# Kernel optimization log

Hardware: AMD Instinct MI355X
Metric: run time of the kernel (lower is better)

The kernel has to match this reference:

```python
import jax, jax.numpy as jnp
import numpy as np

N_NODES = 50000
N_EDGES = 1000000
DIM = 3
NV = 32  # n_vec_in
NS = 32  # n_scalar_in


def setup_inputs() -> dict:
    key = jax.random.key(0)
    ks = jax.random.split(key, 16)
    inp = {
        "xn": jax.random.normal(ks[0], (N_NODES, DIM, NV), dtype=jnp.float32),
        "xn_attr": jax.random.normal(ks[1], (N_NODES, NS), dtype=jnp.float32),
        "xe_attr": jax.random.normal(ks[2], (N_EDGES,), dtype=jnp.float32),
        "xe_src": jax.random.randint(ks[3], (N_EDGES,), 0, N_NODES),
        "xe_dst": jax.random.randint(ks[4], (N_EDGES,), 0, N_NODES),
        # MixVecScalar params
        "ms_M": jax.random.normal(ks[5], (NV, NS), dtype=jnp.float32),
        "ms_w": jax.random.normal(ks[6], (1,), dtype=jnp.float32),
        # fc1 / fc2: Linear(1, NV) -> weight [NV] (flattened [NV,1]), bias [NV]
        "fc1_w": jax.random.normal(ks[7], (NV,), dtype=jnp.float32),
        "fc1_b": jax.random.normal(ks[8], (NV,), dtype=jnp.float32),
        "fc2_w": jax.random.normal(ks[9], (NV,), dtype=jnp.float32),
        "fc2_b": jax.random.normal(ks[10], (NV,), dtype=jnp.float32),
        # NodesToEdges MixVecVec
        "n2e_M1": jax.random.normal(ks[11], (NV, NV), dtype=jnp.float32),
        "n2e_M2": jax.random.normal(ks[12], (NV, NV), dtype=jnp.float32),
        # standalone MixVecVec
        "vv_M1": jax.random.normal(ks[13], (NV, NV), dtype=jnp.float32),
        "vv_M2": jax.random.normal(ks[14], (NV, NV), dtype=jnp.float32),
        # EdgesToNodes MixVecVec
        "e2n_M1": jax.random.normal(jax.random.fold_in(key, 101), (NV, NV), dtype=jnp.float32),
        "e2n_M2": jax.random.normal(jax.random.fold_in(key, 102), (NV, NV), dtype=jnp.float32),
    }
    return inp


def reference(xn, xn_attr, xe_attr, xe_src, xe_dst,
              ms_M, ms_w, fc1_w, fc1_b, fc2_w, fc2_b,
              n2e_M1, n2e_M2, vv_M1, vv_M2, e2n_M1, e2n_M2):
    n_nodes = xn.shape[0]

    # MixVecScalar: x3 = ((xn @ M) * xn_attr[:,None,:]) @ M.T; blend by angle
    x3 = jnp.einsum('ndv,vs->nds', xn, ms_M) * xn_attr[:, None, :]
    x3 = jnp.einsum('nds,vs->ndv', x3, ms_M)
    angle = 0.1 * ms_w  # shape [1]
    xn = jnp.cos(angle) * xn + jnp.sin(angle) * x3

    # fc1: silu(Linear(1->NV)(xe_attr))  -> per-edge weight [E, NV]
    W1 = jax.nn.silu(xe_attr[:, None] * fc1_w[None, :] + fc1_b[None, :])

    # NodesToEdges: gather, weight, mix
    xs = xn[xe_src]  # [E, DIM, NV]
    xd = xn[xe_dst]
    xe_grad = W1[:, None, :] * (xs - xd)
    xe_ave = W1[:, None, :] * (xs + xd) / 2.0
    xe = (jnp.einsum('edv,vw->edw', xe_grad, n2e_M1)
          + jnp.einsum('edv,vw->edw', xe_ave, n2e_M2)) / 2.0

    # MixVecVec(xe, xe) = xe @ (M1 + M2) / 2
    xe = jnp.einsum('edv,vw->edw', xe, (vv_M1 + vv_M2) / 2.0)

    # fc2 weight
    W2 = jax.nn.silu(xe_attr[:, None] * fc2_w[None, :] + fc2_b[None, :])

    # EdgesToNodes: weighted scatter-add to dst and src, then mix
    wxe = W2[:, None, :] * xe  # [E, DIM, NV]
    xn_1 = jax.ops.segment_sum(wxe, xe_dst, num_segments=n_nodes)
    xn_2 = jax.ops.segment_sum(wxe, xe_src, num_segments=n_nodes)
    xn_div = xn_1 - xn_2
    xn_ave = xn_1 + xn_2
    xn = (jnp.einsum('ndv,vw->ndw', xn_div, e2n_M1)
          + jnp.einsum('ndv,vw->ndw', xn_ave, e2n_M2)) / 2.0

    # ActivationVec: x * tanh(||x||_dim1)
    xnorm = jnp.linalg.norm(xn, axis=1)  # [N, NV]
    xn = xn * jnp.tanh(xnorm)[:, None, :]
    return xn
```

## Files before the change

### kernel.cpp

```cpp
#include <hip/hip_runtime.h>
#include <math.h>


typedef __attribute__((ext_vector_type(8))) short bf16x8;
typedef __attribute__((ext_vector_type(4))) float f32x4;

__device__ __forceinline__ float silu_f(float x) { return x / (1.0f + __expf(-x)); }

__device__ __forceinline__ unsigned cvt_pk_bf16(float lo, float hi) {
  unsigned r;
  asm("v_cvt_pk_bf16_f32 %0, %1, %2" : "=v"(r) : "v"(lo), "v"(hi));
  return r;
}
__device__ __forceinline__ float bf_lo(unsigned w) { return __uint_as_float(w << 16); }
__device__ __forceinline__ float bf_hi(unsigned w) { return __uint_as_float(w & 0xFFFF0000u); }

__global__ __launch_bounds__(1024) void prep_mats_kernel(
    const float* __restrict__ n2e_M1, const float* __restrict__ n2e_M2,
    const float* __restrict__ vv_M1, const float* __restrict__ vv_M2,
    const float* __restrict__ e2n_M1, const float* __restrict__ e2n_M2,
    float* __restrict__ PQRS) {
  __shared__ float Mvv[32][32];
  int j = threadIdx.x & 31, i = threadIdx.x >> 5;
  Mvv[i][j] = 0.5f * (vv_M1[i * 32 + j] + vv_M2[i * 32 + j]);
  __syncthreads();
  float c1 = 0.f, c2 = 0.f;
#pragma unroll
  for (int k = 0; k < 32; k++) {
    c1 += n2e_M1[i * 32 + k] * Mvv[k][j];
    c2 += n2e_M2[i * 32 + k] * Mvv[k][j];
  }
  c1 *= 0.5f;
  c2 *= 0.25f;
  PQRS[0 * 1024 + i * 32 + j] = c1 + c2;
  PQRS[1 * 1024 + i * 32 + j] = c2 - c1;
  PQRS[2 * 1024 + i * 32 + j] = 0.5f * (e2n_M1[i * 32 + j] + e2n_M2[i * 32 + j]);
  PQRS[3 * 1024 + i * 32 + j] = 0.5f * (e2n_M2[i * 32 + j] - e2n_M1[i * 32 + j]);
}

__global__ __launch_bounds__(256) void node_premix_kernel(
    const float* __restrict__ xn, const float* __restrict__ xn_attr,
    const float* __restrict__ ms_M, const float* __restrict__ ms_w,
    unsigned short* __restrict__ xn2b, int n_nodes) {
  __shared__ float M[32][33];
  for (int idx = threadIdx.x; idx < 1024; idx += blockDim.x)
    M[idx >> 5][idx & 31] = ms_M[idx];
  __syncthreads();

  int lane = threadIdx.x & 31;
  int grp = blockIdx.x * (blockDim.x >> 5) + (threadIdx.x >> 5);
  if (grp >= n_nodes) return;

  float angle = 0.1f * ms_w[0];
  float ca = cosf(angle), sa = sinf(angle);

  const float* xp = xn + (size_t)grp * 96;
  float x0 = xp[lane], x1 = xp[32 + lane], x2 = xp[64 + lane];

  float t0 = 0.f, t1 = 0.f, t2 = 0.f;
#pragma unroll
  for (int v = 0; v < 32; v++) {
    float m = M[v][lane];
    t0 += __shfl(x0, v, 32) * m;
    t1 += __shfl(x1, v, 32) * m;
    t2 += __shfl(x2, v, 32) * m;
  }
  float attr = xn_attr[(size_t)grp * 32 + lane];
  t0 *= attr; t1 *= attr; t2 *= attr;

  float y0 = 0.f, y1 = 0.f, y2 = 0.f;
#pragma unroll
  for (int s = 0; s < 32; s++) {
    float m = M[lane][s];
    y0 += __shfl(t0, s, 32) * m;
    y1 += __shfl(t1, s, 32) * m;
    y2 += __shfl(t2, s, 32) * m;
  }

  unsigned short* op = xn2b + (size_t)grp * 96;
  op[lane]      = (unsigned short)cvt_pk_bf16(ca * x0 + sa * y0, 0.f);
  op[32 + lane] = (unsigned short)cvt_pk_bf16(ca * x1 + sa * y1, 0.f);
  op[64 + lane] = (unsigned short)cvt_pk_bf16(ca * x2 + sa * y2, 0.f);
}

__global__ __launch_bounds__(256) void edge_mfma_kernel(
    const unsigned short* __restrict__ xn2b, const float* __restrict__ xe_attr,
    const int* __restrict__ xe_src, const int* __restrict__ xe_dst,
    const float* __restrict__ fc1_w, const float* __restrict__ fc1_b,
    const float* __restrict__ fc2_w, const float* __restrict__ fc2_b,
    const float* __restrict__ Pg, const float* __restrict__ Qg,
    float* __restrict__ acc1, float* __restrict__ acc2, int n_edges) {
  int lane = threadIdx.x & 63;
  int row16 = lane & 15;
  int koct = lane >> 4;

  union { unsigned u[4]; bf16x8 v; } PB0, PB1, QB0, QB1;
#pragma unroll
  for (int w = 0; w < 4; w++) {
    int k0 = koct * 8 + 2 * w;
    PB0.u[w] = cvt_pk_bf16(Pg[k0 * 32 + row16],      Pg[(k0 + 1) * 32 + row16]);
    PB1.u[w] = cvt_pk_bf16(Pg[k0 * 32 + row16 + 16], Pg[(k0 + 1) * 32 + row16 + 16]);
    QB0.u[w] = cvt_pk_bf16(Qg[k0 * 32 + row16],      Qg[(k0 + 1) * 32 + row16]);
    QB1.u[w] = cvt_pk_bf16(Qg[k0 * 32 + row16 + 16], Qg[(k0 + 1) * 32 + row16 + 16]);
  }

  float f1wj[8], f1bj[8];
#pragma unroll
  for (int j = 0; j < 8; j++) {
    f1wj[j] = fc1_w[koct * 8 + j];
    f1bj[j] = fc1_b[koct * 8 + j];
  }
  float f2w0 = fc2_w[row16], f2b0 = fc2_b[row16];
  float f2w1 = fc2_w[row16 + 16], f2b1 = fc2_b[row16 + 16];

  int wid = blockIdx.x * (blockDim.x >> 6) + (threadIdx.x >> 6);
  int wstride = gridDim.x * (blockDim.x >> 6);
  int ntiles = (n_edges + 15) >> 4;

  for (int t = wid; t < ntiles; t += wstride) {
    int ebase = t << 4;
    int e = ebase + row16;
    int ec = e < n_edges ? e : n_edges - 1;
    int sn = xe_src[ec], dn = xe_dst[ec];
    float ea = xe_attr[ec];

    float w1[8];
#pragma unroll
    for (int j = 0; j < 8; j++) w1[j] = silu_f(ea * f1wj[j] + f1bj[j]);

    f32x4 c[3][2];
#pragma unroll
    for (int d = 0; d < 3; d++) {
      c[d][0] = f32x4{0.f, 0.f, 0.f, 0.f};
      c[d][1] = f32x4{0.f, 0.f, 0.f, 0.f};
    }

#pragma unroll
    for (int d = 0; d < 3; d++) {
      uint4 aw = *(const uint4*)(xn2b + (size_t)sn * 96 + d * 32 + koct * 8);
      uint4 bw = *(const uint4*)(xn2b + (size_t)dn * 96 + d * 32 + koct * 8);
      unsigned awa[4] = {aw.x, aw.y, aw.z, aw.w};
      unsigned bwa[4] = {bw.x, bw.y, bw.z, bw.w};
      union { unsigned u[4]; bf16x8 v; } AF, BF;
#pragma unroll
      for (int w = 0; w < 4; w++) {
        AF.u[w] = cvt_pk_bf16(bf_lo(awa[w]) * w1[2 * w], bf_hi(awa[w]) * w1[2 * w + 1]);
        BF.u[w] = cvt_pk_bf16(bf_lo(bwa[w]) * w1[2 * w], bf_hi(bwa[w]) * w1[2 * w + 1]);
      }
      c[d][0] = __builtin_amdgcn_mfma_f32_16x16x32_bf16(AF.v, PB0.v, c[d][0], 0, 0, 0);
      c[d][0] = __builtin_amdgcn_mfma_f32_16x16x32_bf16(BF.v, QB0.v, c[d][0], 0, 0, 0);
      c[d][1] = __builtin_amdgcn_mfma_f32_16x16x32_bf16(AF.v, PB1.v, c[d][1], 0, 0, 0);
      c[d][1] = __builtin_amdgcn_mfma_f32_16x16x32_bf16(BF.v, QB1.v, c[d][1], 0, 0, 0);
    }

    float w2a[4], w2b[4];
    int sn2[4], dn2[4], ev2[4];
#pragma unroll
    for (int rr = 0; rr < 4; rr++) {
      int rp = koct * 4 + rr;
      float ea2 = __shfl(ea, rp, 16);
      sn2[rr] = __shfl(sn, rp, 16);
      dn2[rr] = __shfl(dn, rp, 16);
      ev2[rr] = (ebase + rp) < n_edges;
      w2a[rr] = silu_f(ea2 * f2w0 + f2b0);
      w2b[rr] = silu_f(ea2 * f2w1 + f2b1);
    }

#pragma unroll
    for (int d = 0; d < 3; d++) {
#pragma unroll
      for (int rr = 0; rr < 4; rr++) {
        if (!ev2[rr]) continue;
        float v0 = c[d][0][rr] * w2a[rr];
        float v1 = c[d][1][rr] * w2b[rr];
        float* a1 = acc1 + (size_t)dn2[rr] * 96 + d * 32 + row16;
        float* a2 = acc2 + (size_t)sn2[rr] * 96 + d * 32 + row16;
        atomicAdd(a1, v0);
        atomicAdd(a2, v0);
        atomicAdd(a1 + 16, v1);
        atomicAdd(a2 + 16, v1);
      }
    }
  }
}

__global__ __launch_bounds__(256) void node_post_kernel(
    const float* __restrict__ acc1, const float* __restrict__ acc2,
    const float* __restrict__ Rg, const float* __restrict__ Sg,
    float* __restrict__ out, int n_nodes) {
  __shared__ float R[32][32], S[32][32];
  for (int idx = threadIdx.x; idx < 1024; idx += blockDim.x) {
    R[idx >> 5][idx & 31] = Rg[idx];
    S[idx >> 5][idx & 31] = Sg[idx];
  }
  __syncthreads();
  int lane = threadIdx.x & 31;
  int grp = blockIdx.x * (blockDim.x >> 5) + (threadIdx.x >> 5);
  if (grp >= n_nodes) return;
  const float* a = acc1 + (size_t)grp * 96;
  const float* b = acc2 + (size_t)grp * 96;
  float a0 = a[lane], a1 = a[32 + lane], a2 = a[64 + lane];
  float b0 = b[lane], b1 = b[32 + lane], b2 = b[64 + lane];
  float y0 = 0.f, y1 = 0.f, y2 = 0.f;
#pragma unroll
  for (int v = 0; v < 32; v++) {
    float r = R[v][lane], s = S[v][lane];
    y0 += __shfl(a0, v, 32) * r + __shfl(b0, v, 32) * s;
    y1 += __shfl(a1, v, 32) * r + __shfl(b1, v, 32) * s;
    y2 += __shfl(a2, v, 32) * r + __shfl(b2, v, 32) * s;
  }
  float nrm = sqrtf(y0 * y0 + y1 * y1 + y2 * y2);
  float t = tanhf(nrm);
  float* op = out + (size_t)grp * 96;
  op[lane]      = y0 * t;
  op[32 + lane] = y1 * t;
  op[64 + lane] = y2 * t;
}

extern "C" void kernel_launch(void* const* d_in, const int* in_sizes, int n_in,
                              void* d_out, int out_size, void* d_ws, size_t ws_size,
                              hipStream_t stream) {
  const float* xn      = (const float*)d_in[0];
  const float* xn_attr = (const float*)d_in[1];
  const float* xe_attr = (const float*)d_in[2];
  const int*   xe_src  = (const int*)d_in[3];
  const int*   xe_dst  = (const int*)d_in[4];
  const float* ms_M    = (const float*)d_in[5];
  const float* ms_w    = (const float*)d_in[6];
  const float* fc1_w   = (const float*)d_in[7];
  const float* fc1_b   = (const float*)d_in[8];
  const float* fc2_w   = (const float*)d_in[9];
  const float* fc2_b   = (const float*)d_in[10];
  const float* n2e_M1  = (const float*)d_in[11];
  const float* n2e_M2  = (const float*)d_in[12];
  const float* vv_M1   = (const float*)d_in[13];
  const float* vv_M2   = (const float*)d_in[14];
  const float* e2n_M1  = (const float*)d_in[15];
  const float* e2n_M2  = (const float*)d_in[16];

  int n_nodes = in_sizes[0] / 96;
  int n_edges = in_sizes[2];

  char* base = (char*)d_ws;
  float* PQRS = (float*)base;
  unsigned short* xn2b = (unsigned short*)(base + 16384);
  float* acc1 = (float*)(base + 16384 + (size_t)n_nodes * 96 * 2);
  float* acc2 = acc1 + (size_t)n_nodes * 96;

  prep_mats_kernel<<<1, 1024, 0, stream>>>(n2e_M1, n2e_M2, vv_M1, vv_M2,
                                           e2n_M1, e2n_M2, PQRS);

  int nblk = (n_nodes + 7) / 8;
  node_premix_kernel<<<nblk, 256, 0, stream>>>(xn, xn_attr, ms_M, ms_w, xn2b, n_nodes);

  hipMemsetAsync(acc1, 0, (size_t)n_nodes * 96 * 2 * sizeof(float), stream);

  edge_mfma_kernel<<<4096, 256, 0, stream>>>(xn2b, xe_attr, xe_src, xe_dst,
                                             fc1_w, fc1_b, fc2_w, fc2_b,
                                             PQRS, PQRS + 1024, acc1, acc2, n_edges);

  node_post_kernel<<<nblk, 256, 0, stream>>>(acc1, acc2, PQRS + 2048, PQRS + 3072,
                                             (float*)d_out, n_nodes);
}
```

Before: 827.2 us.

## Accumulate edge scatter in bf16 with packed atomics and transposed MFMA output

Switches the node accumulators from fp32 to bf16 and scatters edge contributions with global_atomic_pk_add_bf16, two values per atomic. The MFMA operands are swapped so each lane holds four consecutive feature columns of one edge, which lets packed atomics target contiguous addresses. The goal is to cut the number of atomic operations and the accumulator footprint and traffic. The cost is precision: summing roughly 40 edge contributions per node in bf16 can build up large rounding error.

```diff
diff --git a/kernel.cpp b/kernel.cpp
--- a/kernel.cpp
+++ b/kernel.cpp
@@ -1,4 +1,5 @@
 #include <hip/hip_runtime.h>
+#include <hip/hip_bf16.h>
 #include <math.h>
 
 
@@ -14,6 +15,10 @@
 }
 __device__ __forceinline__ float bf_lo(unsigned w) { return __uint_as_float(w << 16); }
 __device__ __forceinline__ float bf_hi(unsigned w) { return __uint_as_float(w & 0xFFFF0000u); }
+
+__device__ __forceinline__ void atomic_pk_add_bf16(unsigned short* p, unsigned d) {
+  asm volatile("global_atomic_pk_add_bf16 %0, %1, off" :: "v"(p), "v"(d) : "memory");
+}
 
 __global__ __launch_bounds__(1024) void prep_mats_kernel(
     const float* __restrict__ n2e_M1, const float* __restrict__ n2e_M2,
@@ -89,19 +94,20 @@
     const float* __restrict__ fc1_w, const float* __restrict__ fc1_b,
     const float* __restrict__ fc2_w, const float* __restrict__ fc2_b,
     const float* __restrict__ Pg, const float* __restrict__ Qg,
-    float* __restrict__ acc1, float* __restrict__ acc2, int n_edges) {
+    unsigned short* __restrict__ acc1, unsigned short* __restrict__ acc2,
+    int n_edges) {
   int lane = threadIdx.x & 63;
   int row16 = lane & 15;
   int koct = lane >> 4;
 
-  union { unsigned u[4]; bf16x8 v; } PB0, PB1, QB0, QB1;
+  union { unsigned u[4]; bf16x8 v; } PA0, PA1, QA0, QA1;
 #pragma unroll
   for (int w = 0; w < 4; w++) {
     int k0 = koct * 8 + 2 * w;
-    PB0.u[w] = cvt_pk_bf16(Pg[k0 * 32 + row16],      Pg[(k0 + 1) * 32 + row16]);
-    PB1.u[w] = cvt_pk_bf16(Pg[k0 * 32 + row16 + 16], Pg[(k0 + 1) * 32 + row16 + 16]);
-    QB0.u[w] = cvt_pk_bf16(Qg[k0 * 32 + row16],      Qg[(k0 + 1) * 32 + row16]);
-    QB1.u[w] = cvt_pk_bf16(Qg[k0 * 32 + row16 + 16], Qg[(k0 + 1) * 32 + row16 + 16]);
+    PA0.u[w] = cvt_pk_bf16(Pg[k0 * 32 + row16],      Pg[(k0 + 1) * 32 + row16]);
+    PA1.u[w] = cvt_pk_bf16(Pg[k0 * 32 + row16 + 16], Pg[(k0 + 1) * 32 + row16 + 16]);
+    QA0.u[w] = cvt_pk_bf16(Qg[k0 * 32 + row16],      Qg[(k0 + 1) * 32 + row16]);
+    QA1.u[w] = cvt_pk_bf16(Qg[k0 * 32 + row16 + 16], Qg[(k0 + 1) * 32 + row16 + 16]);
   }
 
   float f1wj[8], f1bj[8];
@@ -110,8 +116,12 @@
     f1wj[j] = fc1_w[koct * 8 + j];
     f1bj[j] = fc1_b[koct * 8 + j];
   }
-  float f2w0 = fc2_w[row16], f2b0 = fc2_b[row16];
-  float f2w1 = fc2_w[row16 + 16], f2b1 = fc2_b[row16 + 16];
+  float f2wv[8], f2bv[8];
+#pragma unroll
+  for (int j = 0; j < 4; j++) {
+    f2wv[j]     = fc2_w[koct * 4 + j];      f2bv[j]     = fc2_b[koct * 4 + j];
+    f2wv[4 + j] = fc2_w[16 + koct * 4 + j]; f2bv[4 + j] = fc2_b[16 + koct * 4 + j];
+  }
 
   int wid = blockIdx.x * (blockDim.x >> 6) + (threadIdx.x >> 6);
   int wstride = gridDim.x * (blockDim.x >> 6);
@@ -128,11 +138,11 @@
 #pragma unroll
     for (int j = 0; j < 8; j++) w1[j] = silu_f(ea * f1wj[j] + f1bj[j]);
 
-    f32x4 c[3][2];
+    f32x4 ct[3][2];
 #pragma unroll
     for (int d = 0; d < 3; d++) {
-      c[d][0] = f32x4{0.f, 0.f, 0.f, 0.f};
-      c[d][1] = f32x4{0.f, 0.f, 0.f, 0.f};
+      ct[d][0] = f32x4{0.f, 0.f, 0.f, 0.f};
+      ct[d][1] = f32x4{0.f, 0.f, 0.f, 0.f};
     }
 
 #pragma unroll
@@ -147,45 +157,40 @@
         AF.u[w] = cvt_pk_bf16(bf_lo(awa[w]) * w1[2 * w], bf_hi(awa[w]) * w1[2 * w + 1]);
         BF.u[w] = cvt_pk_bf16(bf_lo(bwa[w]) * w1[2 * w], bf_hi(bwa[w]) * w1[2 * w + 1]);
       }
-      c[d][0] = __builtin_amdgcn_mfma_f32_16x16x32_bf16(AF.v, PB0.v, c[d][0], 0, 0, 0);
-      c[d][0] = __builtin_amdgcn_mfma_f32_16x16x32_bf16(BF.v, QB0.v, c[d][0], 0, 0, 0);
-      c[d][1] = __builtin_amdgcn_mfma_f32_16x16x32_bf16(AF.v, PB1.v, c[d][1], 0, 0, 0);
-      c[d][1] = __builtin_amdgcn_mfma_f32_16x16x32_bf16(BF.v, QB1.v, c[d][1], 0, 0, 0);
+      ct[d][0] = __builtin_amdgcn_mfma_f32_16x16x32_bf16(PA0.v, AF.v, ct[d][0], 0, 0, 0);
+      ct[d][0] = __builtin_amdgcn_mfma_f32_16x16x32_bf16(QA0.v, BF.v, ct[d][0], 0, 0, 0);
+      ct[d][1] = __builtin_amdgcn_mfma_f32_16x16x32_bf16(PA1.v, AF.v, ct[d][1], 0, 0, 0);
+      ct[d][1] = __builtin_amdgcn_mfma_f32_16x16x32_bf16(QA1.v, BF.v, ct[d][1], 0, 0, 0);
     }
 
-    float w2a[4], w2b[4];
-    int sn2[4], dn2[4], ev2[4];
-#pragma unroll
-    for (int rr = 0; rr < 4; rr++) {
-      int rp = koct * 4 + rr;
-      float ea2 = __shfl(ea, rp, 16);
-      sn2[rr] = __shfl(sn, rp, 16);
-      dn2[rr] = __shfl(dn, rp, 16);
-      ev2[rr] = (ebase + rp) < n_edges;
-      w2a[rr] = silu_f(ea2 * f2w0 + f2b0);
-      w2b[rr] = silu_f(ea2 * f2w1 + f2b1);
-    }
-
-#pragma unroll
-    for (int d = 0; d < 3; d++) {
-#pragma unroll
-      for (int rr = 0; rr < 4; rr++) {
-        if (!ev2[rr]) continue;
-        float v0 = c[d][0][rr] * w2a[rr];
-        float v1 = c[d][1][rr] * w2b[rr];
-        float* a1 = acc1 + (size_t)dn2[rr] * 96 + d * 32 + row16;
-        float* a2 = acc2 + (size_t)sn2[rr] * 96 + d * 32 + row16;
-        atomicAdd(a1, v0);
-        atomicAdd(a2, v0);
-        atomicAdd(a1 + 16, v1);
-        atomicAdd(a2 + 16, v1);
+    if (e < n_edges) {
+      float w2v[8];
+#pragma unroll
+      for (int j = 0; j < 8; j++) w2v[j] = silu_f(ea * f2wv[j] + f2bv[j]);
+
+      size_t offD = (size_t)dn * 96;
+      size_t offS = (size_t)sn * 96;
+#pragma unroll
+      for (int d = 0; d < 3; d++) {
+#pragma unroll
+        for (int tt = 0; tt < 2; tt++) {
+          int vo = d * 32 + tt * 16 + koct * 4;
+          unsigned u0 = cvt_pk_bf16(ct[d][tt][0] * w2v[tt * 4 + 0],
+                                    ct[d][tt][1] * w2v[tt * 4 + 1]);
+          unsigned u1 = cvt_pk_bf16(ct[d][tt][2] * w2v[tt * 4 + 2],
+                                    ct[d][tt][3] * w2v[tt * 4 + 3]);
+          atomic_pk_add_bf16(acc1 + offD + vo, u0);
+          atomic_pk_add_bf16(acc1 + offD + vo + 2, u1);
+          atomic_pk_add_bf16(acc2 + offS + vo, u0);
+          atomic_pk_add_bf16(acc2 + offS + vo + 2, u1);
+        }
       }
     }
   }
 }
 
 __global__ __launch_bounds__(256) void node_post_kernel(
-    const float* __restrict__ acc1, const float* __restrict__ acc2,
+    const __hip_bfloat16* __restrict__ acc1, const __hip_bfloat16* __restrict__ acc2,
     const float* __restrict__ Rg, const float* __restrict__ Sg,
     float* __restrict__ out, int n_nodes) {
   __shared__ float R[32][32], S[32][32];
@@ -197,10 +202,14 @@
   int lane = threadIdx.x & 31;
   int grp = blockIdx.x * (blockDim.x >> 5) + (threadIdx.x >> 5);
   if (grp >= n_nodes) return;
-  const float* a = acc1 + (size_t)grp * 96;
-  const float* b = acc2 + (size_t)grp * 96;
-  float a0 = a[lane], a1 = a[32 + lane], a2 = a[64 + lane];
-  float b0 = b[lane], b1 = b[32 + lane], b2 = b[64 + lane];
+  const __hip_bfloat16* a = acc1 + (size_t)grp * 96;
+  const __hip_bfloat16* b = acc2 + (size_t)grp * 96;
+  float a0 = __bfloat162float(a[lane]);
+  float a1 = __bfloat162float(a[32 + lane]);
+  float a2 = __bfloat162float(a[64 + lane]);
+  float b0 = __bfloat162float(b[lane]);
+  float b1 = __bfloat162float(b[32 + lane]);
+  float b2 = __bfloat162float(b[64 + lane]);
   float y0 = 0.f, y1 = 0.f, y2 = 0.f;
 #pragma unroll
   for (int v = 0; v < 32; v++) {
@@ -244,8 +253,8 @@
   char* base = (char*)d_ws;
   float* PQRS = (float*)base;
   unsigned short* xn2b = (unsigned short*)(base + 16384);
-  float* acc1 = (float*)(base + 16384 + (size_t)n_nodes * 96 * 2);
-  float* acc2 = acc1 + (size_t)n_nodes * 96;
+  unsigned short* acc1 = (unsigned short*)(base + 16384 + (size_t)n_nodes * 96 * 2);
+  unsigned short* acc2 = acc1 + (size_t)n_nodes * 96;
 
   prep_mats_kernel<<<1, 1024, 0, stream>>>(n2e_M1, n2e_M2, vv_M1, vv_M2,
                                            e2n_M1, e2n_M2, PQRS);
@@ -253,12 +262,13 @@
   int nblk = (n_nodes + 7) / 8;
   node_premix_kernel<<<nblk, 256, 0, stream>>>(xn, xn_attr, ms_M, ms_w, xn2b, n_nodes);
 
-  hipMemsetAsync(acc1, 0, (size_t)n_nodes * 96 * 2 * sizeof(float), stream);
+  hipMemsetAsync(acc1, 0, (size_t)n_nodes * 96 * 2 * sizeof(unsigned short), stream);
 
   edge_mfma_kernel<<<4096, 256, 0, stream>>>(xn2b, xe_attr, xe_src, xe_dst,
                                              fc1_w, fc1_b, fc2_w, fc2_b,
                                              PQRS, PQRS + 1024, acc1, acc2, n_edges);
 
-  node_post_kernel<<<nblk, 256, 0, stream>>>(acc1, acc2, PQRS + 2048, PQRS + 3072,
+  node_post_kernel<<<nblk, 256, 0, stream>>>((__hip_bfloat16*)acc1, (__hip_bfloat16*)acc2,
+                                             PQRS + 2048, PQRS + 3072,
                                              (float*)d_out, n_nodes);
 }
```

Result: slower. 1.438 ms (+73.8%).
